# Kernel tuning notes

Hardware: AMD Instinct MI355X
Metric: run time of the kernel (lower is better)

## Reference

```python
import jax, jax.numpy as jnp
import numpy as np

I_SIZE = 4096
H_SIZE = 2048
WIN = 10          # window_size
MAX_DEPTH = 6
EPS = 1e-9


def setup_inputs() -> dict:
    key = jax.random.key(0)
    ks = jax.random.split(key, 10)
    u = lambda k, s: jax.random.uniform(k, s, dtype=jnp.float32)
    n = lambda k, s: jax.random.normal(k, s, dtype=jnp.float32) * 0.02
    return {
        "input": u(ks[0], (WIN, I_SIZE)),
        "stack": u(ks[1], (1, H_SIZE, I_SIZE)),
        "stack_pointer": u(ks[2], (1, H_SIZE)),
        "input_pointer": u(ks[3], (1, WIN + 1)),
        "ff_w": n(ks[4], (I_SIZE, I_SIZE)), "ff_b": jnp.zeros((I_SIZE,), jnp.float32),
        "gate_w": n(ks[5], (2, 1)), "gate_b": jnp.zeros((2,), jnp.float32),
        "kin_w": n(ks[6], (I_SIZE, 2 * I_SIZE)), "kin_b": jnp.zeros((I_SIZE,), jnp.float32),
        "kouth_w": n(ks[7], (I_SIZE, I_SIZE)), "kouth_b": jnp.zeros((I_SIZE,), jnp.float32),
        "kouti_w": n(ks[8], (I_SIZE, I_SIZE)), "kouti_b": jnp.zeros((I_SIZE,), jnp.float32),
    }


def _forward(input, stack, stack_pointer, input_pointer,
             ff_w, ff_b, gate_w, gate_b, kin_w, kin_b,
             kouth_w, kouth_b, kouti_w, kouti_b):
    lsm = jax.nn.log_softmax
    lin = lambda x, w, b: jnp.matmul(x, w.T) + b

    def push(vec, stk, ptr):
        # stk: [1,H,I], ptr: [1,H], vec: [1,I] or [1,1,I]
        stk = stk * (1.0 - ptr)[..., None] + jnp.matmul(ptr[..., None], vec)
        ptr_new = jnp.concatenate([jnp.zeros((ptr.shape[0], 1), ptr.dtype), ptr[:, :-1]], axis=-1)
        return stk, ptr_new

    def pop(stk, ptr):
        ptr_new = jnp.concatenate([ptr[:, 1:], jnp.zeros((ptr.shape[0], 1), ptr.dtype)], axis=-1)
        s = jnp.sum(ptr_new, -1)                      # [1]
        norm = jnp.where(s > 0, ptr_new / jnp.where(s > 0, s, 1.0), ptr_new)
        outvec = jnp.matmul(norm, stk)                # [1,1,I]
        stk_new = (1.0 - ptr_new)[..., None] * stk
        ptr_new = ptr_new.at[:, 0].add(ptr[:, 0])
        return outvec, stk_new, ptr_new

    def get(inp, ptr):
        outvec = jnp.matmul(ptr[:, :-1], inp)         # [1,I]
        ptr_new = jnp.concatenate([jnp.zeros((ptr.shape[0], 1), ptr.dtype), ptr[:, :-1]], axis=-1)
        ptr_new = ptr_new.at[:, -1].add(ptr[:, -1])
        return outvec, ptr_new

    def kld(p, q):
        p = p + EPS
        q = q + EPS
        p = p / jnp.sum(p)
        q = q / jnp.sum(q)
        return jnp.sum(p * jnp.log(p / q))

    def calforward(invec, hvec):
        predvec = lsm(lin(hvec, ff_w, ff_b))
        perp_pred = kld(predvec, invec)
        inp_cat = jnp.concatenate([invec.reshape(1, 1, -1), hvec.reshape(1, 1, -1)], axis=-1)
        new_inp = jnp.exp(lsm(lin(inp_cat, kin_w, kin_b)))      # softmax, [1,1,I]
        proj_hvec = jnp.exp(lsm(lin(new_inp, kouth_w, kouth_b)))
        proj_invec = jnp.exp(lsm(lin(new_inp, kouti_w, kouti_b)))
        perp = perp_pred + kld(proj_invec, invec) / 2 + kld(proj_hvec, hvec) / 2
        gate = jnp.exp(lsm(lin(perp_pred.reshape(1), gate_w, gate_b)))  # [2]
        gate = jnp.where(jnp.sum(hvec) == 0, jnp.array([1.0, 0.0], gate.dtype),
                         jnp.where(jnp.sum(invec) == 0, jnp.array([0.0, 1.0], gate.dtype), gate))
        return gate, perp, new_inp

    stackmem, sptrmem, iptrmem, wldl, perps = [], [], [], [], []
    for ii in range(MAX_DEPTH):
        if ii == 0:
            invec, st1, sp1 = pop(stack, stack_pointer)
            hvec, st1, sp1 = pop(st1, sp1)
            gate, perp, new_inp = calforward(invec, hvec)
            st1, sp1 = push(new_inp, st1, sp1)
            stackmem.append(st1); sptrmem.append(sp1); iptrmem.append(input_pointer)
            wldl.append(gate[1]); perps.append(perp)
        else:
            ip2, st2, sp2 = input_pointer, stack, stack_pointer
            for _ in range(ii - 1):
                invec, ip2 = get(input, ip2)
                st2, sp2 = push(invec, st2, sp2)
            invec, ip2 = get(input, ip2)
            hvec, st2, sp2 = pop(st2, sp2)
            gate, perp, new_inp = calforward(invec, hvec)
            st2, sp2 = push(new_inp, st2, sp2)
            stackmem.append(st2); sptrmem.append(sp2); iptrmem.append(ip2)
            input_avail = 1.0 - ip2[0, -1]
            wldl.append((1.0 - wldl[ii - 1]) * gate[1] * input_avail)
            perps.append(perp)

    w = jnp.stack(wldl)
    w = w / jnp.sum(w)
    resperp = jnp.sum(w * jnp.stack(perps))
    new_stack = sum(w[i] * stackmem[i] for i in range(MAX_DEPTH))
    new_sp = sum(w[i] * sptrmem[i] for i in range(MAX_DEPTH))
    new_ip = sum(w[i] * iptrmem[i] for i in range(MAX_DEPTH))
    ssum = jnp.sum(new_sp, -1, keepdims=True)
    new_sp = jnp.where(ssum > 0, new_sp / jnp.where(ssum > 0, ssum, 1.0), new_sp)
    isum = jnp.sum(new_ip, -1, keepdims=True)
    new_ip = jnp.where(isum > 0, new_ip / jnp.where(isum > 0, isum, 1.0), new_ip)
    return resperp, new_stack, new_sp, new_ip


def reference(input, stack, stack_pointer, input_pointer,
              ff_w, ff_b, gate_w, gate_b, kin_w, kin_b,
              kouth_w, kouth_b, kouti_w, kouti_b):
    return _forward(input, stack, stack_pointer, input_pointer,
                    ff_w, ff_b, gate_w, gate_b, kin_w, kin_b,
                    kouth_w, kouth_b, kouti_w, kouti_b)
```

## Files before the change

### kernel.cpp

```cpp
#include <hip/hip_runtime.h>
#include <cfloat>
#include <cmath>

#define HH   2048
#define ISZ  4096
#define WN   10
#define ND   6
#define EPSF 1e-9f

#define O_WROW   0
#define O_GETW   14336
#define O_POPC   14464
#define O_AVAIL  14496
#define O_SCAL   14528
#define O_IPTR   14592
#define O_DFIN   14720
#define O_CNEW   27008
#define O_CFIN   39296
#define O_SPTR   88448
#define O_NEWINP 100736
#define O_G      125312
#define O_HVEC   145792
#define O_IVEC   170368
#define O_RPART  317824
#define O_PZ     1235328
#define O_PYFF   1431936
#define O_PYH    1530240
#define O_PYI    1628544

__device__ __forceinline__ float blockReduceSum(float v, float* sm){
  int ln = threadIdx.x & 63, w = threadIdx.x >> 6;
  #pragma unroll
  for (int o=32;o>0;o>>=1) v += __shfl_down(v,o);
  if (ln==0) sm[w]=v;
  __syncthreads();
  if (threadIdx.x==0){
    float r=0.f; int nw=(int)(blockDim.x>>6);
    for (int i=0;i<nw;i++) r+=sm[i];
    sm[16]=r;
  }
  __syncthreads();
  float r = sm[16];
  __syncthreads();
  return r;
}

template<int N>
__device__ __forceinline__ void bRedSumN(float* v, float* sm){
  int ln=threadIdx.x&63, w=threadIdx.x>>6;
  #pragma unroll
  for (int o=32;o>0;o>>=1){
    #pragma unroll
    for (int i=0;i<N;i++) v[i]+=__shfl_down(v[i],o);
  }
  if (ln==0){ for (int i=0;i<N;i++) sm[w*N+i]=v[i]; }
  __syncthreads();
  if (threadIdx.x==0){
    for (int i=0;i<N;i++){ float r=0.f; for (int q=0;q<16;q++) r+=sm[q*N+i]; sm[16*N+i]=r; }
  }
  __syncthreads();
  for (int i=0;i<N;i++) v[i]=sm[16*N+i];
  __syncthreads();
}

template<int N>
__device__ __forceinline__ void bRedMaxN(float* v, float* sm){
  int ln=threadIdx.x&63, w=threadIdx.x>>6;
  #pragma unroll
  for (int o=32;o>0;o>>=1){
    #pragma unroll
    for (int i=0;i<N;i++) v[i]=fmaxf(v[i],__shfl_down(v[i],o));
  }
  if (ln==0){ for (int i=0;i<N;i++) sm[w*N+i]=v[i]; }
  __syncthreads();
  if (threadIdx.x==0){
    for (int i=0;i<N;i++){ float r=-FLT_MAX; for (int q=0;q<16;q++) r=fmaxf(r,sm[q*N+i]); sm[16*N+i]=r; }
  }
  __syncthreads();
  for (int i=0;i<N;i++) v[i]=sm[16*N+i];
  __syncthreads();
}

__global__ __launch_bounds__(1024) void k_ptr_prep(
    const float* __restrict__ sp0g, const float* __restrict__ ip0g,
    float* __restrict__ ws)
{
  __shared__ float sp[HH], q[HH], D[HH];
  __shared__ float c[4][HH];
  __shared__ float red[17];
  const int d   = blockIdx.x;
  const int tid = threadIdx.x;

  float* Wrow = ws + O_WROW;
  float* getW = ws + O_GETW;
  float* popc = ws + O_POPC;
  float* Dfin = ws + O_DFIN;
  float* cnew = ws + O_CNEW;
  float* cfin = ws + O_CFIN;
  float* sptr = ws + O_SPTR;
  float* iptr = ws + O_IPTR;
  float* avail= ws + O_AVAIL;

  if (d==0 && tid==0){
    float ip[WN+1], nip[WN+1];
    for (int k=0;k<=WN;k++) ip[k]=ip0g[k];
    for (int k=0;k<=WN;k++) iptr[k]=ip[k];
    avail[0] = 1.f - ip[WN];
    for (int t=0;t<5;t++){
      for (int k=0;k<WN;k++) getW[t*16+k]=ip[k];
      nip[0]=0.f;
      for (int k=1;k<=WN;k++) nip[k]=ip[k-1];
      nip[WN] += ip[WN];
      for (int k=0;k<=WN;k++) ip[k]=nip[k];
      for (int k=0;k<=WN;k++) iptr[(t+1)*16+k]=ip[k];
      avail[t+1] = 1.f - ip[WN];
    }
  }

  #pragma unroll
  for (int jj=0;jj<2;jj++){ int j=tid+jj*1024; sp[j]=sp0g[j]; D[j]=1.f; }
  __syncthreads();

  if (d==0){
    #pragma unroll
    for (int jj=0;jj<2;jj++){ int j=tid+jj*1024; q[j]=(j<HH-1)? sp[j+1]:0.f; }
    float ls=0.f;
    #pragma unroll
    for (int jj=0;jj<2;jj++) ls += q[tid+jj*1024];
    float s = blockReduceSum(ls, red);
    float sc = (s>0.f)? 1.f/s : 1.f;
    #pragma unroll
    for (int jj=0;jj<2;jj++){
      int j=tid+jj*1024;
      float qq=q[j];
      Wrow[j] = qq*sc;
      D[j] = 1.f - qq;
      sp[j] = qq + ((j==0)? sp[0] : 0.f);
    }
    __syncthreads();
    #pragma unroll
    for (int jj=0;jj<2;jj++){ int j=tid+jj*1024; q[j]=(j<HH-1)? sp[j+1]:0.f; }
    ls=0.f;
    #pragma unroll
    for (int jj=0;jj<2;jj++) ls += q[tid+jj*1024];
    s = blockReduceSum(ls, red);
    sc = (s>0.f)? 1.f/s : 1.f;
    #pragma unroll
    for (int jj=0;jj<2;jj++){
      int j=tid+jj*1024;
      float qq=q[j];
      Wrow[HH+j] = qq*sc*D[j];
      D[j] *= (1.f-qq);
      sp[j] = qq + ((j==0)? sp[0] : 0.f);
    }
    __syncthreads();
    #pragma unroll
    for (int jj=0;jj<2;jj++){
      int j=tid+jj*1024;
      float p=sp[j];
      Dfin[j] = D[j]*(1.f-p);
      cnew[j] = p;
      sptr[j] = (j==0)? 0.f : sp[j-1];
    }
  } else {
    const int nterms = d-1;
    for (int t=0;t<nterms;t++){
      #pragma unroll
      for (int jj=0;jj<2;jj++){
        int j=tid+jj*1024;
        float p=sp[j], f=1.f-p;
        D[j]*=f;
        for (int u=0;u<t;u++) c[u][j]*=f;
        c[t][j]=p;
      }
      __syncthreads();
      float sv[2];
      #pragma unroll
      for (int jj=0;jj<2;jj++){ int j=tid+jj*1024; sv[jj]=(j==0)?0.f:sp[j-1]; }
      __syncthreads();
      #pragma unroll
      for (int jj=0;jj<2;jj++){ int j=tid+jj*1024; sp[j]=sv[jj]; }
      __syncthreads();
    }
    #pragma unroll
    for (int jj=0;jj<2;jj++){ int j=tid+jj*1024; q[j]=(j<HH-1)? sp[j+1]:0.f; }
    float ls=0.f;
    #pragma unroll
    for (int jj=0;jj<2;jj++) ls += q[tid+jj*1024];
    float s = blockReduceSum(ls, red);
    float sc = (s>0.f)? 1.f/s : 1.f;
    for (int t=0;t<nterms;t++){
      float pc=0.f;
      #pragma unroll
      for (int jj=0;jj<2;jj++){ int j=tid+jj*1024; pc += q[j]*sc*c[t][j]; }
      pc = blockReduceSum(pc, red);
      if (tid==0) popc[d*4+t]=pc;
    }
    #pragma unroll
    for (int jj=0;jj<2;jj++){
      int j=tid+jj*1024;
      float qq=q[j];
      Wrow[(1+d)*HH+j] = qq*sc*D[j];
      float f = 1.f-qq;
      D[j] *= f;
      for (int t=0;t<nterms;t++) c[t][j] *= f;
      sp[j] = qq + ((j==0)? sp[0] : 0.f);
    }
    __syncthreads();
    #pragma unroll
    for (int jj=0;jj<2;jj++){
      int j=tid+jj*1024;
      float p=sp[j], f=1.f-p;
      Dfin[d*HH+j] = D[j]*f;
      for (int t=0;t<nterms;t++) cfin[(d*4+t)*HH+j] = c[t][j]*f;
      cnew[d*HH+j] = p;
      sptr[d*HH+j] = (j==0)? 0.f : sp[j-1];
    }
  }
}

__global__ __launch_bounds__(256) void k_rowsum(
    const float* __restrict__ stk, const float* __restrict__ wrow,
    float* __restrict__ Rp)
{
  __shared__ float wsh[7][64];
  const int col = blockIdx.x*256 + threadIdx.x;
  const int by  = blockIdx.y;
  const int r0  = by*64;
  for (int idx=threadIdx.x; idx<7*64; idx+=256){
    int k=idx>>6, r=idx&63;
    wsh[k][r]=wrow[k*HH + r0 + r];
  }
  __syncthreads();
  float a0=0,a1=0,a2=0,a3=0,a4=0,a5=0,a6=0;
  const float* sp = stk + (size_t)r0*ISZ + col;
  #pragma unroll 4
  for (int r=0;r<64;r++){
    float v = sp[(size_t)r*ISZ];
    a0+=wsh[0][r]*v; a1+=wsh[1][r]*v; a2+=wsh[2][r]*v; a3+=wsh[3][r]*v;
    a4+=wsh[4][r]*v; a5+=wsh[5][r]*v; a6+=wsh[6][r]*v;
  }
  Rp[(size_t)(by*7+0)*ISZ+col]=a0; Rp[(size_t)(by*7+1)*ISZ+col]=a1;
  Rp[(size_t)(by*7+2)*ISZ+col]=a2; Rp[(size_t)(by*7+3)*ISZ+col]=a3;
  Rp[(size_t)(by*7+4)*ISZ+col]=a4; Rp[(size_t)(by*7+5)*ISZ+col]=a5;
  Rp[(size_t)(by*7+6)*ISZ+col]=a6;
}

__global__ __launch_bounds__(128) void k_hv(
    const float* __restrict__ input, float* __restrict__ ws)
{
  __shared__ float gwS[80], pcS[24];
  const int tid=threadIdx.x;
  const int cx = blockIdx.x*128 + tid;
  if (tid<80) gwS[tid]=ws[O_GETW+tid];
  if (tid<24) pcS[tid]=ws[O_POPC+tid];
  __syncthreads();
  float inp[WN];
  #pragma unroll
  for (int k=0;k<WN;k++) inp[k]=input[k*ISZ+cx];
  float g[5];
  #pragma unroll
  for (int t=0;t<5;t++){
    float a=0.f;
    #pragma unroll
    for (int k=0;k<WN;k++) a += gwS[t*16+k]*inp[k];
    g[t]=a;
    ws[O_G + t*ISZ + cx]=a;
  }
  float R[7];
  #pragma unroll
  for (int k=0;k<7;k++){
    float a=0.f;
    for (int y=0;y<32;y++) a += ws[O_RPART + (size_t)(y*7+k)*ISZ + cx];
    R[k]=a;
  }
  ws[O_IVEC + cx]=R[0];
  ws[O_HVEC + cx]=R[1];
  #pragma unroll
  for (int d=1;d<ND;d++){
    ws[O_IVEC + d*ISZ + cx] = g[d-1];
    float h = R[1+d];
    for (int t=0;t<=d-2;t++) h += pcS[d*4+t]*g[t];
    ws[O_HVEC + d*ISZ + cx] = h;
  }
}

__device__ __forceinline__ void mv_chunk(
    const float* __restrict__ W, int ldw, int wcol0,
    const float* __restrict__ Xg, const float* __restrict__ bias,
    float* __restrict__ Yp, int rb, int chunk, float4* xs4)
{
  const float4* X4 = (const float4*)Xg;
  for (int idx=threadIdx.x; idx<6*256; idx+=256){
    int d = idx>>8, j = idx&255;
    xs4[idx] = X4[d*1024 + chunk*256 + j];
  }
  __syncthreads();
  const int wv = threadIdx.x>>6, ln = threadIdx.x&63;
  const int row0 = rb*32 + wv*8;
  const float* wr = W + (size_t)row0*ldw + wcol0 + chunk*1024;
  float acc[8][6];
  #pragma unroll
  for (int r=0;r<8;r++)
    #pragma unroll
    for (int d=0;d<6;d++) acc[r][d]=0.f;

  #pragma unroll 1
  for (int i=0;i<4;i++){
    const int k = ln*4 + i*256;
    float4 w4[8];
    #pragma unroll
    for (int r=0;r<8;r++) w4[r] = *(const float4*)(wr + (size_t)r*ldw + k);
    float4 x4[6];
    #pragma unroll
    for (int d=0;d<6;d++) x4[d] = xs4[d*256 + ln + i*64];
    #pragma unroll
    for (int r=0;r<8;r++){
      #pragma unroll
      for (int d=0;d<6;d++){
        acc[r][d] += w4[r].x*x4[d].x + w4[r].y*x4[d].y
                   + w4[r].z*x4[d].z + w4[r].w*x4[d].w;
      }
    }
  }
  #pragma unroll
  for (int r=0;r<8;r++){
    #pragma unroll
    for (int d=0;d<6;d++){
      float v = acc[r][d];
      #pragma unroll
      for (int o=32;o>0;o>>=1) v += __shfl_down(v,o);
      if (ln==0) Yp[d*ISZ + row0 + r] = v + (bias ? bias[row0+r] : 0.f);
    }
  }
}

__global__ __launch_bounds__(256) void k_matvecA(
    const float* __restrict__ ff_w, const float* __restrict__ ff_b,
    const float* __restrict__ kin_w, const float* __restrict__ kin_b,
    float* __restrict__ ws)
{
  __shared__ float4 xs4[6*256];
  const int t = blockIdx.x >> 9;
  const int rem = blockIdx.x & 511;
  const int chunk = rem >> 7;
  const int rb = rem & 127;
  if (t==0)
    mv_chunk(kin_w, 2*ISZ, 0,   ws+O_IVEC, (chunk==0)?kin_b:nullptr,
             ws+O_PZ   + chunk*6*ISZ, rb, chunk, xs4);
  else if (t==1)
    mv_chunk(ff_w,  ISZ,   0,   ws+O_HVEC, (chunk==0)?ff_b:nullptr,
             ws+O_PYFF + chunk*6*ISZ, rb, chunk, xs4);
  else
    mv_chunk(kin_w, 2*ISZ, ISZ, ws+O_HVEC, nullptr,
             ws+O_PZ   + (4+chunk)*6*ISZ, rb, chunk, xs4);
}

__global__ __launch_bounds__(256) void k_matvecB(
    const float* __restrict__ kouth_w, const float* __restrict__ kouth_b,
    const float* __restrict__ kouti_w, const float* __restrict__ kouti_b,
    float* __restrict__ ws)
{
  __shared__ float4 xs4[6*256];
  const int t = blockIdx.x >> 9;
  const int rem = blockIdx.x & 511;
  const int chunk = rem >> 7;
  const int rb = rem & 127;
  if (t==0)
    mv_chunk(kouth_w, ISZ, 0, ws+O_NEWINP, (chunk==0)?kouth_b:nullptr,
             ws+O_PYH + chunk*6*ISZ, rb, chunk, xs4);
  else
    mv_chunk(kouti_w, ISZ, 0, ws+O_NEWINP, (chunk==0)?kouti_b:nullptr,
             ws+O_PYI + chunk*6*ISZ, rb, chunk, xs4);
}

__global__ __launch_bounds__(1024) void k_s1(
    const float* __restrict__ gate_w, const float* __restrict__ gate_b,
    float* __restrict__ ws)
{
  __shared__ float sm[96];
  const int d=blockIdx.x, tid=threadIdx.x;
  const float* iv = ws+O_IVEC+ d*ISZ;
  const float* hv = ws+O_HVEC+ d*ISZ;

  float yv[4], zv[4], ivv[4], hvv[4];
  #pragma unroll
  for (int i=0;i<4;i++){
    int cx=tid+i*1024;
    float y=0.f, z=0.f;
    #pragma unroll
    for (int s=0;s<4;s++) y += ws[O_PYFF + (s*6+d)*ISZ + cx];
    #pragma unroll
    for (int s=0;s<8;s++) z += ws[O_PZ   + (s*6+d)*ISZ + cx];
    yv[i]=y; zv[i]=z; ivv[i]=iv[cx]; hvv[i]=hv[cx];
  }
  float mx[2]={-FLT_MAX,-FLT_MAX};
  #pragma unroll
  for (int i=0;i<4;i++){ mx[0]=fmaxf(mx[0],yv[i]); mx[1]=fmaxf(mx[1],zv[i]); }
  bRedMaxN<2>(mx,sm);

  float s5[5]={0,0,0,0,0};
  #pragma unroll
  for (int i=0;i<4;i++){
    s5[0]+=expf(yv[i]-mx[0]); s5[1]+=expf(zv[i]-mx[1]);
    s5[2]+=yv[i]; s5[3]+=ivv[i]; s5[4]+=hvv[i];
  }
  bRedSumN<5>(s5,sm);
  const float lse = mx[0]+logf(s5[0]);
  const float sP  = s5[2] - (float)ISZ*lse + (float)ISZ*EPSF;
  const float sQ  = s5[3] + (float)ISZ*EPSF;
  const float inv2= 1.f/s5[1];

  float kk[1]={0.f};
  #pragma unroll
  for (int i=0;i<4;i++){
    int cx=tid+i*1024;
    ws[O_NEWINP + d*ISZ + cx] = expf(zv[i]-mx[1])*inv2;
    float ph=((yv[i]-lse)+EPSF)/sP;
    float qh=(ivv[i]+EPSF)/sQ;
    kk[0]+=ph*(logf(ph)-logf(qh));
  }
  bRedSumN<1>(kk,sm);

  if (tid==0){
    float pp=kk[0];
    float a0=gate_w[0]*pp+gate_b[0];
    float a1=gate_w[1]*pp+gate_b[1];
    float mg=fmaxf(a0,a1);
    float e0=expf(a0-mg), e1=expf(a1-mg);
    float g1=e1/(e0+e1);
    if (s5[4]==0.f) g1=0.f;
    else if (s5[3]==0.f) g1=1.f;
    ws[O_SCAL+d]=pp; ws[O_SCAL+6+d]=g1;
    ws[O_SCAL+24+d]=sQ;
    ws[O_SCAL+30+d]=s5[4]+(float)ISZ*EPSF;
  }
}

__global__ __launch_bounds__(1024) void k_s2(float* __restrict__ ws)
{
  __shared__ float sm[96];
  const int d=blockIdx.x, tid=threadIdx.x;
  const float* hv = ws+O_HVEC+ d*ISZ;
  const float* iv = ws+O_IVEC+ d*ISZ;

  float yhv[4], yiv[4], hvv[4], ivv[4];
  #pragma unroll
  for (int i=0;i<4;i++){
    int cx=tid+i*1024;
    float yh=0.f, yi=0.f;
    #pragma unroll
    for (int s=0;s<4;s++){
      yh += ws[O_PYH + (s*6+d)*ISZ + cx];
      yi += ws[O_PYI + (s*6+d)*ISZ + cx];
    }
    yhv[i]=yh; yiv[i]=yi; hvv[i]=hv[cx]; ivv[i]=iv[cx];
  }
  float mx[2]={-FLT_MAX,-FLT_MAX};
  #pragma unroll
  for (int i=0;i<4;i++){ mx[0]=fmaxf(mx[0],yhv[i]); mx[1]=fmaxf(mx[1],yiv[i]); }
  bRedMaxN<2>(mx,sm);
  float se[2]={0,0};
  #pragma unroll
  for (int i=0;i<4;i++){ se[0]+=expf(yhv[i]-mx[0]); se[1]+=expf(yiv[i]-mx[1]); }
  bRedSumN<2>(se,sm);
  const float invh=1.f/se[0], invi=1.f/se[1];
  const float spc = 1.f + (float)ISZ*EPSF;
  const float sqh = ws[O_SCAL+30+d], sqi = ws[O_SCAL+24+d];

  float kk[2]={0,0};
  #pragma unroll
  for (int i=0;i<4;i++){
    float ph=(expf(yhv[i]-mx[0])*invh+EPSF)/spc;
    float qh=(hvv[i]+EPSF)/sqh;
    kk[0]+=ph*(logf(ph)-logf(qh));
    float pi=(expf(yiv[i]-mx[1])*invi+EPSF)/spc;
    float qi=(ivv[i]+EPSF)/sqi;
    kk[1]+=pi*(logf(pi)-logf(qi));
  }
  bRedSumN<2>(kk,sm);
  if (tid==0) ws[O_SCAL+12+d] = ws[O_SCAL+d] + 0.5f*(kk[0]+kk[1]);
}

__global__ __launch_bounds__(1024) void k_fin(float* __restrict__ ws,
                                              float* __restrict__ out)
{
  __shared__ float sm[32];
  __shared__ float wsh[ND];
  const int tid=threadIdx.x;
  if (tid==0){
    const float* g1=ws+O_SCAL+6; const float* pp=ws+O_SCAL+12; const float* av=ws+O_AVAIL;
    float wl[ND]; wl[0]=g1[0];
    for (int i=1;i<ND;i++) wl[i]=(1.f-wl[i-1])*g1[i]*av[i];
    float s=0.f; for (int i=0;i<ND;i++) s+=wl[i];
    float rp=0.f;
    for (int i=0;i<ND;i++){ float wn=wl[i]/s; wsh[i]=wn; rp+=wn*pp[i]; }
    out[0]=rp;
  }
  __syncthreads();
  float w[ND];
  #pragma unroll
  for (int dd=0;dd<ND;dd++) w[dd]=wsh[dd];
  const float* sptr=ws+O_SPTR;
  float snl[2], ms=0.f;
  #pragma unroll
  for (int jj=0;jj<2;jj++){
    int j=tid+jj*1024;
    float sn=0.f;
    #pragma unroll
    for (int dd=0;dd<ND;dd++) sn += w[dd]*sptr[dd*HH+j];
    snl[jj]=sn; ms+=sn;
  }
  float t[1]={ms};
  bRedSumN<1>(t,sm);
  float ssum=t[0];
  #pragma unroll
  for (int jj=0;jj<2;jj++){
    int j=tid+jj*1024;
    out[1 + (size_t)HH*ISZ + j] = (ssum>0.f)? snl[jj]/ssum : snl[jj];
  }
  if (tid==0){
    const float* iptr=ws+O_IPTR;
    float ipn[WN+1]; float is=0.f;
    for (int k=0;k<=WN;k++){
      float a=0.f;
      for (int dd=0;dd<ND;dd++) a += w[dd]*iptr[dd*16+k];
      ipn[k]=a; is+=a;
    }
    size_t base = 1 + (size_t)HH*ISZ + HH;
    for (int k=0;k<=WN;k++) out[base+k] = (is>0.f)? ipn[k]/is : ipn[k];
  }
}

__global__ __launch_bounds__(256) void k_stack_out(
    const float* __restrict__ stk, const float* __restrict__ ws,
    float* __restrict__ out)
{
  __shared__ float Vt[10*1024];
  __shared__ float wsh[ND];
  __shared__ float mwS[8];
  __shared__ float ceS[8][10];
  const int tid=threadIdx.x;
  const int c0 = blockIdx.x*1024;
  const int j0 = blockIdx.y*8;

  if (tid==0){
    const float* g1=ws+O_SCAL+6; const float* av=ws+O_AVAIL;
    float wl[ND]; wl[0]=g1[0];
    for (int i=1;i<ND;i++) wl[i]=(1.f-wl[i-1])*g1[i]*av[i];
    float s=0.f; for (int i=0;i<ND;i++) s+=wl[i];
    for (int i=0;i<ND;i++) wsh[i]=wl[i]/s;
  }
  const float* V = ws+O_NEWINP;
  for (int idx=tid; idx<10*1024; idx+=256){
    int v=idx>>10, cc=idx&1023;
    Vt[idx] = V[v*ISZ + c0 + cc];
  }
  __syncthreads();
  if (tid<8){
    int j=j0+tid;
    float mw=0.f, ce[10]={0,0,0,0,0,0,0,0,0,0};
    for (int dd=0;dd<ND;dd++){
      float wd=wsh[dd];
      mw    += wd*ws[O_DFIN+dd*HH+j];
      ce[dd] = wd*ws[O_CNEW+dd*HH+j];
    }
    for (int t=0;t<4;t++){
      float a=0.f;
      for (int dd=t+2;dd<ND;dd++) a += wsh[dd]*ws[O_CFIN+(dd*4+t)*HH+j];
      ce[6+t]=a;
    }
    mwS[tid]=mw;
    for (int v=0;v<10;v++) ceS[tid][v]=ce[v];
  }
  __syncthreads();
  const int tx4 = tid*4;
  for (int r=0;r<8;r++){
    int j=j0+r;
    float mw = mwS[r];
    float4 sv = *(const float4*)(stk + (size_t)j*ISZ + c0 + tx4);
    float o0 = mw*sv.x, o1 = mw*sv.y, o2 = mw*sv.z, o3 = mw*sv.w;
    #pragma unroll
    for (int v=0;v<10;v++){
      const float* vr = Vt + v*1024 + tx4;
      float cv=ceS[r][v];
      o0 += cv*vr[0]; o1 += cv*vr[1]; o2 += cv*vr[2]; o3 += cv*vr[3];
    }
    float* op = out + 1 + (size_t)j*ISZ + c0 + tx4;
    op[0]=o0; op[1]=o1; op[2]=o2; op[3]=o3;
  }
}

extern "C" void kernel_launch(void* const* d_in, const int* in_sizes, int n_in,
                              void* d_out, int out_size, void* d_ws, size_t ws_size,
                              hipStream_t stream)
{
  (void)in_sizes; (void)n_in; (void)out_size; (void)ws_size;
  const float* input   = (const float*)d_in[0];
  const float* stack   = (const float*)d_in[1];
  const float* sp0     = (const float*)d_in[2];
  const float* ip0     = (const float*)d_in[3];
  const float* ff_w    = (const float*)d_in[4];
  const float* ff_b    = (const float*)d_in[5];
  const float* gate_w  = (const float*)d_in[6];
  const float* gate_b  = (const float*)d_in[7];
  const float* kin_w   = (const float*)d_in[8];
  const float* kin_b   = (const float*)d_in[9];
  const float* kouth_w = (const float*)d_in[10];
  const float* kouth_b = (const float*)d_in[11];
  const float* kouti_w = (const float*)d_in[12];
  const float* kouti_b = (const float*)d_in[13];
  float* out = (float*)d_out;
  float* ws  = (float*)d_ws;

  k_ptr_prep<<<ND,1024,0,stream>>>(sp0, ip0, ws);
  k_rowsum<<<dim3(16,32),256,0,stream>>>(stack, ws+O_WROW, ws+O_RPART);
  k_hv<<<32,128,0,stream>>>(input, ws);
  k_matvecA<<<1536,256,0,stream>>>(ff_w, ff_b, kin_w, kin_b, ws);
  k_s1<<<ND,1024,0,stream>>>(gate_w, gate_b, ws);
  k_matvecB<<<1024,256,0,stream>>>(kouth_w, kouth_b, kouti_w, kouti_b, ws);
  k_s2<<<ND,1024,0,stream>>>(ws);
  k_stack_out<<<dim3(4,256),256,0,stream>>>(stack, ws, out);
  k_fin<<<1,1024,0,stream>>>(ws, out);
}
```

Measured before the change: 229.7 us.

## Stream matvec weights into LDS with double-buffered async global_load_lds

Replaces the register-loaded weight and x reads in the batched matvec kernels with async global_load_lds copies into a double-buffered LDS stage. While one k-slice is being computed, the next slice is prefetched, and explicit vmcnt waits plus barriers order the two. The aim is to overlap HBM latency with FMA work in these memory-bound matvecs. In exchange the kernels use much more LDS (about 76KB per block), which may lower occupancy, and correctness now depends on hand-counted vmcnt values.

```diff
diff --git a/kernel.cpp b/kernel.cpp
--- a/kernel.cpp
+++ b/kernel.cpp
@@ -285,44 +285,68 @@
   }
 }
 
-__device__ __forceinline__ void mv_chunk(
+#define WOFF(b,row) ((b)*8192 + (row)*256)
+#define XOFF(b,d)   (16384 + (b)*1536 + (d)*256)
+
+__device__ __forceinline__ void gl_lds(const float* g, float* l){
+  __builtin_amdgcn_global_load_lds(
+      (const __attribute__((address_space(1))) void*)g,
+      (__attribute__((address_space(3))) void*)l, 16, 0, 0);
+}
+
+__device__ __forceinline__ void mv_stream(
     const float* __restrict__ W, int ldw, int wcol0,
     const float* __restrict__ Xg, const float* __restrict__ bias,
-    float* __restrict__ Yp, int rb, int chunk, float4* xs4)
-{
-  const float4* X4 = (const float4*)Xg;
-  for (int idx=threadIdx.x; idx<6*256; idx+=256){
-    int d = idx>>8, j = idx&255;
-    xs4[idx] = X4[d*1024 + chunk*256 + j];
-  }
-  __syncthreads();
+    float* __restrict__ Yp, int rb, int chunk, float* lds)
+{
   const int wv = threadIdx.x>>6, ln = threadIdx.x&63;
-  const int row0 = rb*32 + wv*8;
-  const float* wr = W + (size_t)row0*ldw + wcol0 + chunk*1024;
+  const int row0 = rb*32;
+  const float* wbase = W + (size_t)row0*ldw + wcol0 + chunk*1024 + ln*4;
+  const float* xbase = Xg + chunk*1024 + ln*4;
+
   float acc[8][6];
   #pragma unroll
   for (int r=0;r<8;r++)
     #pragma unroll
     for (int d=0;d<6;d++) acc[r][d]=0.f;
 
-  #pragma unroll 1
-  for (int i=0;i<4;i++){
-    const int k = ln*4 + i*256;
-    float4 w4[8];
-    #pragma unroll
-    for (int r=0;r<8;r++) w4[r] = *(const float4*)(wr + (size_t)r*ldw + k);
-    float4 x4[6];
-    #pragma unroll
-    for (int d=0;d<6;d++) x4[d] = xs4[d*256 + ln + i*64];
+  auto STAGE = [&](int sc, int b){
+    const float* wp = wbase + sc*256;
+    #pragma unroll
+    for (int r=0;r<8;r++)
+      gl_lds(wp + (size_t)(wv*8+r)*ldw, lds + WOFF(b, wv*8+r));
+    for (int d=wv; d<6; d+=4)
+      gl_lds(xbase + d*ISZ + sc*256, lds + XOFF(b,d));
+  };
+
+  STAGE(0,0);
+  for (int c=0;c<4;c++){
+    const int b = c&1;
+    if (c<3){
+      STAGE(c+1, b^1);
+      if (wv<2) asm volatile("s_waitcnt vmcnt(10)" ::: "memory");
+      else      asm volatile("s_waitcnt vmcnt(9)"  ::: "memory");
+    } else {
+      asm volatile("s_waitcnt vmcnt(0)" ::: "memory");
+    }
+    __builtin_amdgcn_sched_barrier(0);
+    __builtin_amdgcn_s_barrier();
+    __builtin_amdgcn_sched_barrier(0);
+    float4 xk[6];
+    #pragma unroll
+    for (int d=0;d<6;d++) xk[d] = *(const float4*)(lds + XOFF(b,d) + ln*4);
     #pragma unroll
     for (int r=0;r<8;r++){
+      float4 w4 = *(const float4*)(lds + WOFF(b, wv*8+r) + ln*4);
       #pragma unroll
       for (int d=0;d<6;d++){
-        acc[r][d] += w4[r].x*x4[d].x + w4[r].y*x4[d].y
-                   + w4[r].z*x4[d].z + w4[r].w*x4[d].w;
+        acc[r][d] += w4.x*xk[d].x + w4.y*xk[d].y + w4.z*xk[d].z + w4.w*xk[d].w;
       }
     }
-  }
+    __builtin_amdgcn_sched_barrier(0);
+    __builtin_amdgcn_s_barrier();
+  }
+
   #pragma unroll
   for (int r=0;r<8;r++){
     #pragma unroll
@@ -330,7 +354,10 @@
       float v = acc[r][d];
       #pragma unroll
       for (int o=32;o>0;o>>=1) v += __shfl_down(v,o);
-      if (ln==0) Yp[d*ISZ + row0 + r] = v + (bias ? bias[row0+r] : 0.f);
+      if (ln==0){
+        int row = row0 + wv*8 + r;
+        Yp[d*ISZ + row] = v + (bias ? bias[row] : 0.f);
+      }
     }
   }
 }
@@ -340,20 +367,20 @@
     const float* __restrict__ kin_w, const float* __restrict__ kin_b,
     float* __restrict__ ws)
 {
-  __shared__ float4 xs4[6*256];
+  __shared__ float lds[19456];
   const int t = blockIdx.x >> 9;
   const int rem = blockIdx.x & 511;
   const int chunk = rem >> 7;
   const int rb = rem & 127;
   if (t==0)
-    mv_chunk(kin_w, 2*ISZ, 0,   ws+O_IVEC, (chunk==0)?kin_b:nullptr,
-             ws+O_PZ   + chunk*6*ISZ, rb, chunk, xs4);
+    mv_stream(kin_w, 2*ISZ, 0,   ws+O_IVEC, (chunk==0)?kin_b:nullptr,
+              ws+O_PZ   + chunk*6*ISZ, rb, chunk, lds);
   else if (t==1)
-    mv_chunk(ff_w,  ISZ,   0,   ws+O_HVEC, (chunk==0)?ff_b:nullptr,
-             ws+O_PYFF + chunk*6*ISZ, rb, chunk, xs4);
+    mv_stream(ff_w,  ISZ,   0,   ws+O_HVEC, (chunk==0)?ff_b:nullptr,
+              ws+O_PYFF + chunk*6*ISZ, rb, chunk, lds);
   else
-    mv_chunk(kin_w, 2*ISZ, ISZ, ws+O_HVEC, nullptr,
-             ws+O_PZ   + (4+chunk)*6*ISZ, rb, chunk, xs4);
+    mv_stream(kin_w, 2*ISZ, ISZ, ws+O_HVEC, nullptr,
+              ws+O_PZ   + (4+chunk)*6*ISZ, rb, chunk, lds);
 }
 
 __global__ __launch_bounds__(256) void k_matvecB(
@@ -361,17 +388,17 @@
     const float* __restrict__ kouti_w, const float* __restrict__ kouti_b,
     float* __restrict__ ws)
 {
-  __shared__ float4 xs4[6*256];
+  __shared__ float lds[19456];
   const int t = blockIdx.x >> 9;
   const int rem = blockIdx.x & 511;
   const int chunk = rem >> 7;
   const int rb = rem & 127;
   if (t==0)
-    mv_chunk(kouth_w, ISZ, 0, ws+O_NEWINP, (chunk==0)?kouth_b:nullptr,
-             ws+O_PYH + chunk*6*ISZ, rb, chunk, xs4);
+    mv_stream(kouth_w, ISZ, 0, ws+O_NEWINP, (chunk==0)?kouth_b:nullptr,
+              ws+O_PYH + chunk*6*ISZ, rb, chunk, lds);
   else
-    mv_chunk(kouti_w, ISZ, 0, ws+O_NEWINP, (chunk==0)?kouti_b:nullptr,
-             ws+O_PYI + chunk*6*ISZ, rb, chunk, xs4);
+    mv_stream(kouti_w, ISZ, 0, ws+O_NEWINP, (chunk==0)?kouti_b:nullptr,
+              ws+O_PYI + chunk*6*ISZ, rb, chunk, lds);
 }
 
 __global__ __launch_bounds__(1024) void k_s1(
```

Result: slower. 247.8 us (+7.9%).
